# Optimization experiments

Hardware: AMD Instinct MI355X
Metric: run time of the kernel (lower is better)

Reference implementation:

```python
import jax, jax.numpy as jnp
import numpy as np

N_NODES = 20000
F_IN = 32
CHANNELS = 32
EDGE_DIM = 8
N_EDGES = 160000
N_PAIRS = 50000
N_OUT = 1


def setup_inputs() -> dict:
    key = jax.random.key(0)
    ks = jax.random.split(key, 12)
    x = jax.random.normal(ks[0], (N_NODES, F_IN), dtype=jnp.float32)
    edge_index = jax.random.randint(ks[1], (N_EDGES, 2), 0, N_NODES, dtype=jnp.int32)
    e = jax.random.uniform(ks[2], (N_EDGES, EDGE_DIM), dtype=jnp.float32)
    idx_a = jax.random.randint(ks[3], (N_PAIRS,), 0, N_NODES, dtype=jnp.int32)
    idx_b = jax.random.randint(ks[4], (N_PAIRS,), 0, N_NODES, dtype=jnp.int32)
    s1 = 1.0 / np.sqrt(EDGE_DIM)
    s2 = 1.0 / np.sqrt(F_IN)
    # ECCConv layer 1: kernel network (edge_dim -> F_in*channels), root weight, bias
    knw1 = jax.random.normal(ks[5], (EDGE_DIM, F_IN * CHANNELS), dtype=jnp.float32) * s1
    knb1 = jnp.zeros((F_IN * CHANNELS,), dtype=jnp.float32)
    root1 = jax.random.normal(ks[6], (F_IN, CHANNELS), dtype=jnp.float32) * s2
    bias1 = jnp.zeros((CHANNELS,), dtype=jnp.float32)
    # ECCConv layer 2
    knw2 = jax.random.normal(ks[7], (EDGE_DIM, CHANNELS * CHANNELS), dtype=jnp.float32) * s1
    knb2 = jnp.zeros((CHANNELS * CHANNELS,), dtype=jnp.float32)
    root2 = jax.random.normal(ks[8], (CHANNELS, CHANNELS), dtype=jnp.float32) * (1.0 / np.sqrt(CHANNELS))
    bias2 = jnp.zeros((CHANNELS,), dtype=jnp.float32)
    # final utility head
    dw = jax.random.normal(ks[9], (CHANNELS, N_OUT), dtype=jnp.float32) * (1.0 / np.sqrt(CHANNELS))
    db = jnp.zeros((N_OUT,), dtype=jnp.float32)
    return {
        "x": x, "e": e,
        "knw1": knw1, "knb1": knb1, "root1": root1, "bias1": bias1,
        "knw2": knw2, "knb2": knb2, "root2": root2, "bias2": bias2,
        "dw": dw, "db": db,
        "edge_index": edge_index, "idx_a": idx_a, "idx_b": idx_b,
    }


def _ecc_conv(x, src, tgt, e, knw, knb, root, bias):
    # per-edge filter: [E, F_in, F_out]
    fin, fout = root.shape
    kernels = (e @ knw + knb).reshape(-1, fin, fout)
    msg = jnp.einsum('ei,eio->eo', x[src], kernels)          # [E, F_out]
    agg = jax.ops.segment_sum(msg, tgt, num_segments=x.shape[0])  # sum aggregate
    return jax.nn.relu(agg + x @ root + bias)


def reference(x, e, knw1, knb1, root1, bias1, knw2, knb2, root2, bias2, dw, db,
              edge_index, idx_a, idx_b):
    src = edge_index[:, 0]
    tgt = edge_index[:, 1]
    h = _ecc_conv(x, src, tgt, e, knw1, knb1, root1, bias1)
    h = _ecc_conv(h, src, tgt, e, knw2, knb2, root2, bias2)
    util = h @ dw + db                # [N, n_out]
    return util[idx_b] - util[idx_a]  # [n_pairs, n_out]
```

## Files before the change

### kernel.cpp

```cpp
#include <hip/hip_runtime.h>

#define N_NODES 20000
#define N_EDGES 160000
#define N_PAIRS 50000
#define DMAX 32

typedef __attribute__((ext_vector_type(8))) short short8v;
typedef __attribute__((ext_vector_type(4))) float f32x4;

__device__ __forceinline__ float bf2f(unsigned int u) {
    return __uint_as_float(u << 16);
}
__device__ __forceinline__ unsigned int f2bf(float f) {
    unsigned int u = __float_as_uint(f);
    u += 0x7fffu + ((u >> 16) & 1u);
    return u >> 16;
}

__global__ __launch_bounds__(256) void prep_kernel(int* __restrict__ cnt,
        const float* __restrict__ knw1, const float* __restrict__ knb1,
        const float* __restrict__ root1, ushort* __restrict__ wf1,
        const float* __restrict__ knw2, const float* __restrict__ knb2,
        const float* __restrict__ root2, ushort* __restrict__ wf2) {
    int b = blockIdx.x, t = threadIdx.x;
    if (b < 79) {
        int idx = b * 256 + t;
        if (idx < N_NODES) cnt[idx] = 0;
        return;
    }
    int u = (b - 79) * 256 + t;
    const float *knw, *knb, *root;
    ushort* wf;
    if (u < 10240) { knw = knw1; knb = knb1; root = root1; wf = wf1; }
    else { u -= 10240; knw = knw2; knb = knb2; root = root2; wf = wf2; }
    int e = u & 7, l = (u >> 3) & 63, rest = u >> 9;
    int ks = rest % 10, nt = rest / 10;
    int k = ks * 32 + ((l >> 4) << 3) + e;
    int o = nt * 16 + (l & 15);
    float v;
    if (k < 256) v = knw[k * 32 + o];
    else if (k < 288) v = knb[(k - 256) * 32 + o];
    else v = root[(k - 288) * 32 + o];
    wf[u] = (ushort)f2bf(v);
}

__global__ __launch_bounds__(256) void fill_adj(const int* __restrict__ ei,
                                                const float* __restrict__ E,
                                                int* __restrict__ cnt,
                                                int* __restrict__ adjsrc,
                                                uint4* __restrict__ adjEb) {
    int e = blockIdx.x * blockDim.x + threadIdx.x;
    if (e >= N_EDGES) return;
    int2 st = ((const int2*)ei)[e];
    int slot = atomicAdd(&cnt[st.y], 1);
    if (slot < DMAX) {
        int idx = (st.y << 5) + slot;
        adjsrc[idx] = st.x;
        const float4* e4 = (const float4*)(E + (size_t)e * 8);
        float4 a = e4[0], b = e4[1];
        uint4 p;
        p.x = f2bf(a.x) | (f2bf(a.y) << 16);
        p.y = f2bf(a.z) | (f2bf(a.w) << 16);
        p.z = f2bf(b.x) | (f2bf(b.y) << 16);
        p.w = f2bf(b.z) | (f2bf(b.w) << 16);
        adjEb[idx] = p;
    }
}

#define EDGE_FMA_P(p, xv)                                                      \
    g0 += bf2f((p).x & 0xffffu) * (xv); g1 += bf2f((p).x >> 16) * (xv);        \
    g2 += bf2f((p).y & 0xffffu) * (xv); g3 += bf2f((p).y >> 16) * (xv);        \
    g4 += bf2f((p).z & 0xffffu) * (xv); g5 += bf2f((p).z >> 16) * (xv);        \
    g6 += bf2f((p).w & 0xffffu) * (xv); g7 += bf2f((p).w >> 16) * (xv);        \
    g8 += (xv);

__global__ __launch_bounds__(256) void edge_gather(const float* __restrict__ X,
                                                   const int* __restrict__ cnt,
                                                   const int* __restrict__ adjsrc,
                                                   const uint4* __restrict__ adjEb,
                                                   float* __restrict__ G) {
    int t = blockIdx.x * blockDim.x + threadIdx.x;
    int n = t >> 6;
    if (n >= N_NODES) return;
    int lane = t & 63;
    int i = lane & 31;
    int half = lane >> 5;

    int deg = min(cnt[n], DMAX);
    int base = n << 5;
    float g0 = 0.f, g1 = 0.f, g2 = 0.f, g3 = 0.f;
    float g4 = 0.f, g5 = 0.f, g6 = 0.f, g7 = 0.f, g8 = 0.f;

    int c = 0;
    for (; c + 8 <= deg; c += 8) {
        int k0 = base + c + half * 4;
        int s0 = adjsrc[k0 + 0];
        int s1 = adjsrc[k0 + 1];
        int s2 = adjsrc[k0 + 2];
        int s3 = adjsrc[k0 + 3];
        uint4 p0 = adjEb[k0 + 0];
        uint4 p1 = adjEb[k0 + 1];
        uint4 p2 = adjEb[k0 + 2];
        uint4 p3 = adjEb[k0 + 3];
        float xv0 = X[s0 * 32 + i];
        float xv1 = X[s1 * 32 + i];
        float xv2 = X[s2 * 32 + i];
        float xv3 = X[s3 * 32 + i];
        EDGE_FMA_P(p0, xv0);
        EDGE_FMA_P(p1, xv1);
        EDGE_FMA_P(p2, xv2);
        EDGE_FMA_P(p3, xv3);
    }
    for (int k = c + half; k < deg; k += 2) {
        int s = adjsrc[base + k];
        uint4 p = adjEb[base + k];
        float xv = X[s * 32 + i];
        EDGE_FMA_P(p, xv);
    }

    g0 += __shfl_xor(g0, 32); g1 += __shfl_xor(g1, 32);
    g2 += __shfl_xor(g2, 32); g3 += __shfl_xor(g3, 32);
    g4 += __shfl_xor(g4, 32); g5 += __shfl_xor(g5, 32);
    g6 += __shfl_xor(g6, 32); g7 += __shfl_xor(g7, 32);
    g8 += __shfl_xor(g8, 32);

    if (half == 0) {
        float* gr = G + (size_t)n * 288;
        gr[0 * 32 + i] = g0; gr[1 * 32 + i] = g1;
        gr[2 * 32 + i] = g2; gr[3 * 32 + i] = g3;
        gr[4 * 32 + i] = g4; gr[5 * 32 + i] = g5;
        gr[6 * 32 + i] = g6; gr[7 * 32 + i] = g7;
        gr[256 + i] = g8;
    }
}

__global__ __launch_bounds__(256) void epi_mfma(const float* __restrict__ G,
                                                const float* __restrict__ X,
                                                const ushort* __restrict__ wfrag,
                                                const float* __restrict__ bias,
                                                const float* __restrict__ dw,
                                                const float* __restrict__ db,
                                                float* __restrict__ H,
                                                float* __restrict__ util,
                                                int mode) {
    int wv = threadIdx.x >> 6;
    int tile = blockIdx.x * 4 + wv;
    if (tile >= N_NODES / 16) return;
    int l = threadIdx.x & 63;
    int row = l & 15, kg = l >> 4;
    int node = tile * 16 + row;

    f32x4 acc0 = {0.f, 0.f, 0.f, 0.f};
    f32x4 acc1 = {0.f, 0.f, 0.f, 0.f};
    const float* gbase = G + (size_t)node * 288 + kg * 8;
    const float* xbase = X + (size_t)node * 32 + kg * 8;

#pragma unroll
    for (int ks = 0; ks < 10; ++ks) {
        const float* src = (ks < 9) ? (gbase + ks * 32) : xbase;
        float4 f0 = *(const float4*)(src);
        float4 f1 = *(const float4*)(src + 4);
        short8v a;
        a[0] = (short)f2bf(f0.x); a[1] = (short)f2bf(f0.y);
        a[2] = (short)f2bf(f0.z); a[3] = (short)f2bf(f0.w);
        a[4] = (short)f2bf(f1.x); a[5] = (short)f2bf(f1.y);
        a[6] = (short)f2bf(f1.z); a[7] = (short)f2bf(f1.w);
        short8v b0 = *(const short8v*)(wfrag + ((0 * 10 + ks) * 64 + l) * 8);
        short8v b1 = *(const short8v*)(wfrag + ((1 * 10 + ks) * 64 + l) * 8);
        acc0 = __builtin_amdgcn_mfma_f32_16x16x32_bf16(a, b0, acc0, 0, 0, 0);
        acc1 = __builtin_amdgcn_mfma_f32_16x16x32_bf16(a, b1, acc1, 0, 0, 0);
    }

    int o0 = l & 15, o1 = 16 + (l & 15);
    int rbase = tile * 16 + kg * 4;
    if (mode == 0) {
#pragma unroll
        for (int v = 0; v < 4; ++v) {
            int n = rbase + v;
            H[n * 32 + o0] = fmaxf(acc0[v] + bias[o0], 0.f);
            H[n * 32 + o1] = fmaxf(acc1[v] + bias[o1], 0.f);
        }
    } else {
        float b0v = bias[o0], b1v = bias[o1];
        float d0 = dw[o0], d1 = dw[o1];
        float dbv = db[0];
#pragma unroll
        for (int v = 0; v < 4; ++v) {
            float p = fmaxf(acc0[v] + b0v, 0.f) * d0
                    + fmaxf(acc1[v] + b1v, 0.f) * d1;
            p += __shfl_xor(p, 1);
            p += __shfl_xor(p, 2);
            p += __shfl_xor(p, 4);
            p += __shfl_xor(p, 8);
            if ((l & 15) == 0) util[rbase + v] = p + dbv;
        }
    }
}

__global__ void pair_kernel(const float* __restrict__ util, const int* __restrict__ ia,
                            const int* __restrict__ ib, float* __restrict__ out) {
    int p = blockIdx.x * blockDim.x + threadIdx.x;
    if (p >= N_PAIRS) return;
    out[p] = util[ib[p]] - util[ia[p]];
}

extern "C" void kernel_launch(void* const* d_in, const int* in_sizes, int n_in,
                              void* d_out, int out_size, void* d_ws, size_t ws_size,
                              hipStream_t stream) {
    const float* x     = (const float*)d_in[0];
    const float* e     = (const float*)d_in[1];
    const float* knw1  = (const float*)d_in[2];
    const float* knb1  = (const float*)d_in[3];
    const float* root1 = (const float*)d_in[4];
    const float* bias1 = (const float*)d_in[5];
    const float* knw2  = (const float*)d_in[6];
    const float* knb2  = (const float*)d_in[7];
    const float* root2 = (const float*)d_in[8];
    const float* bias2 = (const float*)d_in[9];
    const float* dw    = (const float*)d_in[10];
    const float* db    = (const float*)d_in[11];
    const int*   ei    = (const int*)d_in[12];
    const int*   ia    = (const int*)d_in[13];
    const int*   ib    = (const int*)d_in[14];
    float* out = (float*)d_out;

    float* ws = (float*)d_ws;
    float*  G      = ws;
    float*  H      = ws + 5760000;
    float*  util   = ws + 6400000;
    int*    cnt    = (int*)(ws + 6420000);
    int*    adjsrc = (int*)(ws + 6440000);
    uint4*  adjEb  = (uint4*)(ws + 7080000);
    ushort* wf1    = (ushort*)(ws + 9640000);
    ushort* wf2    = (ushort*)(ws + 9645120);

    int nblk_epi = (N_NODES / 16 + 3) / 4;
    int nblk_gat = (N_NODES * 64) / 256;

    prep_kernel<<<159, 256, 0, stream>>>(cnt, knw1, knb1, root1, wf1,
                                         knw2, knb2, root2, wf2);
    fill_adj<<<(N_EDGES + 255) / 256, 256, 0, stream>>>(ei, e, cnt, adjsrc, adjEb);

    edge_gather<<<nblk_gat, 256, 0, stream>>>(x, cnt, adjsrc, adjEb, G);
    epi_mfma<<<nblk_epi, 256, 0, stream>>>(G, x, wf1, bias1, dw, db, H, util, 0);

    edge_gather<<<nblk_gat, 256, 0, stream>>>(H, cnt, adjsrc, adjEb, G);
    epi_mfma<<<nblk_epi, 256, 0, stream>>>(G, H, wf2, bias2, dw, db, H, util, 1);

    pair_kernel<<<(N_PAIRS + 255) / 256, 256, 0, stream>>>(util, ia, ib, out);
}
```

Measured before the change: 68.73 us.

## Store gathered intermediate as bf16 in MFMA fragment layout

```diff
diff --git a/kernel.cpp b/kernel.cpp
--- a/kernel.cpp
+++ b/kernel.cpp
@@ -78,7 +78,7 @@
                                                    const int* __restrict__ cnt,
                                                    const int* __restrict__ adjsrc,
                                                    const uint4* __restrict__ adjEb,
-                                                   float* __restrict__ G) {
+                                                   ushort* __restrict__ Gb) {
     int t = blockIdx.x * blockDim.x + threadIdx.x;
     int n = t >> 6;
     if (n >= N_NODES) return;
@@ -125,17 +125,23 @@
     g8 += __shfl_xor(g8, 32);
 
     if (half == 0) {
-        float* gr = G + (size_t)n * 288;
-        gr[0 * 32 + i] = g0; gr[1 * 32 + i] = g1;
-        gr[2 * 32 + i] = g2; gr[3 * 32 + i] = g3;
-        gr[4 * 32 + i] = g4; gr[5 * 32 + i] = g5;
-        gr[6 * 32 + i] = g6; gr[7 * 32 + i] = g7;
-        gr[256 + i] = g8;
-    }
-}
-
-__global__ __launch_bounds__(256) void epi_mfma(const float* __restrict__ G,
-                                                const float* __restrict__ X,
+        float xself = X[n * 32 + i];
+        size_t tb = (size_t)(n >> 4) * 10 * 512;
+        int off = (((i >> 3) << 4) | (n & 15)) * 8 + (i & 7);
+        Gb[tb + 0 * 512 + off] = (ushort)f2bf(g0);
+        Gb[tb + 1 * 512 + off] = (ushort)f2bf(g1);
+        Gb[tb + 2 * 512 + off] = (ushort)f2bf(g2);
+        Gb[tb + 3 * 512 + off] = (ushort)f2bf(g3);
+        Gb[tb + 4 * 512 + off] = (ushort)f2bf(g4);
+        Gb[tb + 5 * 512 + off] = (ushort)f2bf(g5);
+        Gb[tb + 6 * 512 + off] = (ushort)f2bf(g6);
+        Gb[tb + 7 * 512 + off] = (ushort)f2bf(g7);
+        Gb[tb + 8 * 512 + off] = (ushort)f2bf(g8);
+        Gb[tb + 9 * 512 + off] = (ushort)f2bf(xself);
+    }
+}
+
+__global__ __launch_bounds__(256) void epi_mfma(const ushort* __restrict__ Gb,
                                                 const ushort* __restrict__ wfrag,
                                                 const float* __restrict__ bias,
                                                 const float* __restrict__ dw,
@@ -147,24 +153,15 @@
     int tile = blockIdx.x * 4 + wv;
     if (tile >= N_NODES / 16) return;
     int l = threadIdx.x & 63;
-    int row = l & 15, kg = l >> 4;
-    int node = tile * 16 + row;
+    int kg = l >> 4;
 
     f32x4 acc0 = {0.f, 0.f, 0.f, 0.f};
     f32x4 acc1 = {0.f, 0.f, 0.f, 0.f};
-    const float* gbase = G + (size_t)node * 288 + kg * 8;
-    const float* xbase = X + (size_t)node * 32 + kg * 8;
+    const ushort* gb = Gb + ((size_t)tile * 10 * 64 + l) * 8;
 
 #pragma unroll
     for (int ks = 0; ks < 10; ++ks) {
-        const float* src = (ks < 9) ? (gbase + ks * 32) : xbase;
-        float4 f0 = *(const float4*)(src);
-        float4 f1 = *(const float4*)(src + 4);
-        short8v a;
-        a[0] = (short)f2bf(f0.x); a[1] = (short)f2bf(f0.y);
-        a[2] = (short)f2bf(f0.z); a[3] = (short)f2bf(f0.w);
-        a[4] = (short)f2bf(f1.x); a[5] = (short)f2bf(f1.y);
-        a[6] = (short)f2bf(f1.z); a[7] = (short)f2bf(f1.w);
+        short8v a = *(const short8v*)(gb + ks * 512);
         short8v b0 = *(const short8v*)(wfrag + ((0 * 10 + ks) * 64 + l) * 8);
         short8v b1 = *(const short8v*)(wfrag + ((1 * 10 + ks) * 64 + l) * 8);
         acc0 = __builtin_amdgcn_mfma_f32_16x16x32_bf16(a, b0, acc0, 0, 0, 0);
@@ -225,14 +222,14 @@
     float* out = (float*)d_out;
 
     float* ws = (float*)d_ws;
-    float*  G      = ws;
-    float*  H      = ws + 5760000;
-    float*  util   = ws + 6400000;
-    int*    cnt    = (int*)(ws + 6420000);
-    int*    adjsrc = (int*)(ws + 6440000);
-    uint4*  adjEb  = (uint4*)(ws + 7080000);
-    ushort* wf1    = (ushort*)(ws + 9640000);
-    ushort* wf2    = (ushort*)(ws + 9645120);
+    ushort* Gb     = (ushort*)ws;
+    float*  H      = ws + 3200000;
+    float*  util   = ws + 3840000;
+    int*    cnt    = (int*)(ws + 3860000);
+    int*    adjsrc = (int*)(ws + 3880000);
+    uint4*  adjEb  = (uint4*)(ws + 4520000);
+    ushort* wf1    = (ushort*)(ws + 7080000);
+    ushort* wf2    = (ushort*)(ws + 7085120);
 
     int nblk_epi = (N_NODES / 16 + 3) / 4;
     int nblk_gat = (N_NODES * 64) / 256;
@@ -241,11 +238,11 @@
                                          knw2, knb2, root2, wf2);
     fill_adj<<<(N_EDGES + 255) / 256, 256, 0, stream>>>(ei, e, cnt, adjsrc, adjEb);
 
-    edge_gather<<<nblk_gat, 256, 0, stream>>>(x, cnt, adjsrc, adjEb, G);
-    epi_mfma<<<nblk_epi, 256, 0, stream>>>(G, x, wf1, bias1, dw, db, H, util, 0);
-
-    edge_gather<<<nblk_gat, 256, 0, stream>>>(H, cnt, adjsrc, adjEb, G);
-    epi_mfma<<<nblk_epi, 256, 0, stream>>>(G, H, wf2, bias2, dw, db, H, util, 1);
+    edge_gather<<<nblk_gat, 256, 0, stream>>>(x, cnt, adjsrc, adjEb, Gb);
+    epi_mfma<<<nblk_epi, 256, 0, stream>>>(Gb, wf1, bias1, dw, db, H, util, 0);
+
+    edge_gather<<<nblk_gat, 256, 0, stream>>>(H, cnt, adjsrc, adjEb, Gb);
+    epi_mfma<<<nblk_epi, 256, 0, stream>>>(Gb, wf2, bias2, dw, db, H, util, 1);
 
     pair_kernel<<<(N_PAIRS + 255) / 256, 256, 0, stream>>>(util, ia, ib, out);
 }
```

After: 59.66 us. 1.15x faster.
